# Performance work log

Hardware: AMD Instinct MI355X
Metric: run time of the kernel (lower is better)

## Reference

```python
import jax, jax.numpy as jnp
import numpy as np

N = 50000
DIM = 64
E = 800000


def setup_inputs() -> dict:
    key = jax.random.key(0)
    ks = jax.random.split(key, 12)
    s = 1.0 / np.sqrt(DIM)
    inp = {
        "x": jax.random.normal(ks[0], (N, DIM), dtype=jnp.float32),
        "coord": jax.random.normal(ks[1], (N, DIM), dtype=jnp.float32),
        "Wq": jax.random.uniform(ks[2], (DIM, DIM), jnp.float32, -s, s),
        "bq": jax.random.uniform(ks[3], (DIM,), jnp.float32, -s, s),
        "Wk": jax.random.uniform(ks[4], (DIM, DIM), jnp.float32, -s, s),
        "bk": jax.random.uniform(ks[5], (DIM,), jnp.float32, -s, s),
        "Wv": jax.random.uniform(ks[6], (DIM, DIM), jnp.float32, -s, s),
        "bv": jax.random.uniform(ks[7], (DIM,), jnp.float32, -s, s),
        "Wc": jax.random.uniform(ks[8], (DIM, 1), jnp.float32, -1.0, 1.0),
        "bc": jax.random.uniform(ks[9], (DIM,), jnp.float32, -1.0, 1.0),
        "edge_index": jax.random.randint(ks[10], (2, E), 0, N, dtype=jnp.int64),
    }
    return inp


def reference(x, coord, Wq, bq, Wk, bk, Wv, bv, Wc, bc, edge_index):
    row, col = edge_index[0], edge_index[1]
    # per-edge coordinate differences and distances: [E, DIM], [E, 1]
    dx = coord[row] - coord[col]
    dist = jnp.linalg.norm(dx, axis=-1, keepdims=True)
    # per-edge QKV projections (torch Linear: x @ W.T + b): [E, DIM]
    q = x[row] @ Wq.T + bq
    k = x[col] @ Wk.T + bk
    v = x[col] @ Wv.T + bv
    # scalar attention logit per edge, GLOBAL softmax over all edges (dim=0)
    attn = jnp.sum(q * k, axis=-1, keepdims=True)  # [E, 1]
    weight = jax.nn.softmax(attn, axis=0)          # [E, 1]
    delta_x = weight * v                            # [E, DIM]
    delta_coord = weight * (dist @ Wc.T + bc) * dx  # [E, DIM]
    # scatter-add back to nodes
    x_out = jax.ops.segment_sum(delta_x, row, num_segments=x.shape[0])
    coord_out = jax.ops.segment_sum(delta_coord, row, num_segments=coord.shape[0])
    return (x + x_out, coord + coord_out)
```

## Files before the change

### kernel.cpp

```cpp
#include <hip/hip_runtime.h>
#include <math.h>

#define N_NODES 50000
#define DIM 64
#define NE 800000
#define NSCAN_BLOCKS ((N_NODES + 255) / 256)
#define NFILL_BLOCKS ((NE + 255) / 256)
#define NQKV_BLOCKS ((N_NODES + 31) / 32)

static __device__ __forceinline__ float bf2f(unsigned short u) {
    return __uint_as_float(((unsigned int)u) << 16);
}
static __device__ __forceinline__ unsigned short f2bf(float f) {
    unsigned int u = __float_as_uint(f);
    u += 0x7fffu + ((u >> 16) & 1u);
    return (unsigned short)(u >> 16);
}

typedef float v2f __attribute__((ext_vector_type(2)));
template <bool HI>
static __device__ __forceinline__ v2f fp8x2(unsigned int u) {
    return __builtin_amdgcn_cvt_pk_f32_fp8((int)u, HI);
}
static __device__ __forceinline__ unsigned char f2fp8(float f) {
    int p = __builtin_amdgcn_cvt_pk_fp8_f32(f, f, 0, false);
    return (unsigned char)(p & 0xff);
}


__global__ __launch_bounds__(256, 5) void k_qkv_fill(
    const float* __restrict__ x, const float* __restrict__ coord,
    const float* __restrict__ Wq, const float* __restrict__ bq,
    const float* __restrict__ Wk, const float* __restrict__ bk,
    const float* __restrict__ Wv, const float* __restrict__ bv,
    const int* __restrict__ eidx, int* __restrict__ cursor,
    int* __restrict__ bucket_col,
    float* __restrict__ Qf, unsigned short* __restrict__ KVC)
{
    __shared__ ushort4 WT2[3][1024];
    __shared__ float4  xs4[32][16];

    if (blockIdx.x < NFILL_BLOCKS) {
        int e = blockIdx.x * 256 + threadIdx.x;
        if (e < NE) {
            int pos = atomicAdd(cursor + eidx[e], 1);
            bucket_col[pos] = eidx[NE + e];
        }
        return;
    }

    const int tid  = threadIdx.x;
    const int base = (blockIdx.x - NFILL_BLOCKS) * 32;
    unsigned char* KVB = (unsigned char*)KVC;

    for (int t = tid; t < 1024; t += 256) {
        int d = t & 63, j2 = t >> 6;
        float4 a = ((const float4*)Wq)[d * 16 + j2];
        float4 b = ((const float4*)Wk)[d * 16 + j2];
        float4 c = ((const float4*)Wv)[d * 16 + j2];
        WT2[0][t] = make_ushort4(f2bf(a.x), f2bf(a.y), f2bf(a.z), f2bf(a.w));
        WT2[1][t] = make_ushort4(f2bf(b.x), f2bf(b.y), f2bf(b.z), f2bf(b.w));
        WT2[2][t] = make_ushort4(f2bf(c.x), f2bf(c.y), f2bf(c.z), f2bf(c.w));
    }
    for (int t = tid; t < 32 * DIM; t += 256) {
        int gn = base + (t >> 6);
        if (gn < N_NODES)
            KVB[(size_t)gn * 256 + 192 + (t & 63)] =
                f2fp8(coord[(size_t)gn * DIM + (t & 63)]);
    }
    for (int t = tid; t < 512; t += 256) {
        int r = t >> 4, j2 = t & 15;
        if (base + r < N_NODES)
            xs4[r][j2] = ((const float4*)x)[(size_t)(base + r) * 16 + j2];
    }
    __syncthreads();

    const int wv = tid >> 6;
    const int d  = tid & 63;
    const float bqv = bq[d], bkv = bk[d], bvv = bv[d];

    float aq[8], ak[8], av[8];
    #pragma unroll
    for (int r = 0; r < 8; ++r) { aq[r] = bqv; ak[r] = bkv; av[r] = bvv; }

    #pragma unroll 4
    for (int j2 = 0; j2 < 16; ++j2) {
        ushort4 uq = WT2[0][j2 * 64 + d];
        ushort4 uk = WT2[1][j2 * 64 + d];
        ushort4 uv = WT2[2][j2 * 64 + d];
        float wqx = bf2f(uq.x), wqy = bf2f(uq.y), wqz = bf2f(uq.z), wqw = bf2f(uq.w);
        float wkx = bf2f(uk.x), wky = bf2f(uk.y), wkz = bf2f(uk.z), wkw = bf2f(uk.w);
        float wvx = bf2f(uv.x), wvy = bf2f(uv.y), wvz = bf2f(uv.z), wvw = bf2f(uv.w);
        #pragma unroll
        for (int r = 0; r < 8; ++r) {
            float4 xv = xs4[wv * 8 + r][j2];
            aq[r] += xv.x * wqx + xv.y * wqy + xv.z * wqz + xv.w * wqw;
            ak[r] += xv.x * wkx + xv.y * wky + xv.z * wkz + xv.w * wkw;
            av[r] += xv.x * wvx + xv.y * wvy + xv.z * wvz + xv.w * wvw;
        }
    }
    #pragma unroll
    for (int r = 0; r < 8; ++r) {
        int n = base + wv * 8 + r;
        if (n < N_NODES) {
            Qf[(size_t)n * DIM + d] = aq[r];
            KVC[(size_t)n * 128 + d]       = f2bf(ak[r]);
            KVB[(size_t)n * 256 + 128 + d] = f2fp8(av[r]);
        }
    }
}

__global__ __launch_bounds__(256) void k_hist(
    const int* __restrict__ eidx, int* __restrict__ counts)
{
    int e = blockIdx.x * 256 + threadIdx.x;
    if (e < NE) atomicAdd(counts + eidx[e], 1);
}

__global__ __launch_bounds__(256) void k_scan1(
    const int* __restrict__ counts, int* __restrict__ offsets,
    int* __restrict__ bsums)
{
    __shared__ int tmp[256];
    int i = blockIdx.x * 256 + threadIdx.x;
    int v = (i < N_NODES) ? counts[i] : 0;
    tmp[threadIdx.x] = v;
    __syncthreads();
    #pragma unroll
    for (int off = 1; off < 256; off <<= 1) {
        int t = (threadIdx.x >= off) ? tmp[threadIdx.x - off] : 0;
        __syncthreads();
        tmp[threadIdx.x] += t;
        __syncthreads();
    }
    if (i < N_NODES) offsets[i] = tmp[threadIdx.x] - v;
    if (threadIdx.x == 255) bsums[blockIdx.x] = tmp[255];
}

__global__ __launch_bounds__(256) void k_scan23(
    int* __restrict__ offsets, int* __restrict__ counts,
    const int* __restrict__ bsums)
{
    __shared__ int red[4];
    const int tid = threadIdx.x;
    const int b   = blockIdx.x;
    int v = (tid < b && tid < NSCAN_BLOCKS) ? bsums[tid] : 0;
    #pragma unroll
    for (int off = 32; off; off >>= 1) v += __shfl_xor(v, off);
    if ((tid & 63) == 0) red[tid >> 6] = v;
    __syncthreads();
    const int pre = red[0] + red[1] + red[2] + red[3];

    int i = b * 256 + tid;
    if (i < N_NODES) {
        int o = offsets[i] + pre;
        offsets[i] = o;
        counts[i]  = o;
    }
    if (i == 0) offsets[N_NODES] = NE;
}

__global__ __launch_bounds__(256) void k_edge_fused(
    const int* __restrict__ bucket_col, const int* __restrict__ offsets,
    const float* __restrict__ Qf, const unsigned short* __restrict__ KVC,
    const float* __restrict__ coord,
    const float* __restrict__ Wc, const float* __restrict__ bc,
    float* __restrict__ out_x, float* __restrict__ out_c,
    float* __restrict__ wsum)
{
    const int lane = threadIdx.x & 63;
    const int n = (blockIdx.x * 256 + threadIdx.x) >> 6;
    if (n >= N_NODES) return;
    const int qt = lane >> 4;
    const int sl = lane & 15;

    const float4 q4  = ((const float4*)Qf)[(size_t)n * 16 + sl];
    const float4 cr4 = ((const float4*)coord)[(size_t)n * 16 + sl];
    const float4 wc4 = ((const float4*)Wc)[sl];
    const float4 bc4 = ((const float4*)bc)[sl];
    const ushort4* K16 = (const ushort4*)KVC;
    const unsigned int* U32 = (const unsigned int*)KVC;

    const int s = offsets[n], t = offsets[n + 1];
    float4 accx = {0.f, 0.f, 0.f, 0.f};
    float4 accc = {0.f, 0.f, 0.f, 0.f};
    float psum = 0.0f;

    for (int base = s; base < t; base += 8) {
        int pos0 = base + qt;
        int pos1 = base + 4 + qt;
        bool v0 = pos0 < t, v1 = pos1 < t;
        int c0 = bucket_col[v0 ? pos0 : (t - 1)];
        int c1 = bucket_col[v1 ? pos1 : (t - 1)];
        ushort4      ku0 = K16[(size_t)c0 * 32 + sl];
        unsigned int vu0 = U32[(size_t)c0 * 64 + 32 + sl];
        unsigned int cu0 = U32[(size_t)c0 * 64 + 48 + sl];
        ushort4      ku1 = K16[(size_t)c1 * 32 + sl];
        unsigned int vu1 = U32[(size_t)c1 * 64 + 32 + sl];
        unsigned int cu1 = U32[(size_t)c1 * 64 + 48 + sl];

        v2f c0a = fp8x2<false>(cu0), c0b = fp8x2<true>(cu0);
        v2f c1a = fp8x2<false>(cu1), c1b = fp8x2<true>(cu1);

        float d0 = q4.x * bf2f(ku0.x) + q4.y * bf2f(ku0.y)
                 + q4.z * bf2f(ku0.z) + q4.w * bf2f(ku0.w);
        float dx0x = cr4.x - c0a.x, dx0y = cr4.y - c0a.y;
        float dx0z = cr4.z - c0b.x, dx0w = cr4.w - c0b.y;
        float e0 = dx0x * dx0x + dx0y * dx0y + dx0z * dx0z + dx0w * dx0w;
        float d1 = q4.x * bf2f(ku1.x) + q4.y * bf2f(ku1.y)
                 + q4.z * bf2f(ku1.z) + q4.w * bf2f(ku1.w);
        float dx1x = cr4.x - c1a.x, dx1y = cr4.y - c1a.y;
        float dx1z = cr4.z - c1b.x, dx1w = cr4.w - c1b.y;
        float e1 = dx1x * dx1x + dx1y * dx1y + dx1z * dx1z + dx1w * dx1w;

        #pragma unroll
        for (int off = 1; off <= 8; off <<= 1) {
            d0 += __shfl_xor(d0, off);
            e0 += __shfl_xor(e0, off);
            d1 += __shfl_xor(d1, off);
            e1 += __shfl_xor(e1, off);
        }
        float p0e = v0 ? __expf(d0) : 0.0f;
        float p1e = v1 ? __expf(d1) : 0.0f;
        float dist0 = sqrtf(e0), dist1 = sqrtf(e1);
        psum += p0e + p1e;

        v2f v0a = fp8x2<false>(vu0), v0b = fp8x2<true>(vu0);
        v2f v1a = fp8x2<false>(vu1), v1b = fp8x2<true>(vu1);
        accx.x += p0e * v0a.x + p1e * v1a.x;
        accx.y += p0e * v0a.y + p1e * v1a.y;
        accx.z += p0e * v0b.x + p1e * v1b.x;
        accx.w += p0e * v0b.y + p1e * v1b.y;
        accc.x += p0e * (dist0 * wc4.x + bc4.x) * dx0x
                + p1e * (dist1 * wc4.x + bc4.x) * dx1x;
        accc.y += p0e * (dist0 * wc4.y + bc4.y) * dx0y
                + p1e * (dist1 * wc4.y + bc4.y) * dx1y;
        accc.z += p0e * (dist0 * wc4.z + bc4.z) * dx0z
                + p1e * (dist1 * wc4.z + bc4.z) * dx1z;
        accc.w += p0e * (dist0 * wc4.w + bc4.w) * dx0w
                + p1e * (dist1 * wc4.w + bc4.w) * dx1w;
    }

    #pragma unroll
    for (int off = 16; off <= 32; off <<= 1) {
        accx.x += __shfl_xor(accx.x, off);
        accx.y += __shfl_xor(accx.y, off);
        accx.z += __shfl_xor(accx.z, off);
        accx.w += __shfl_xor(accx.w, off);
        accc.x += __shfl_xor(accc.x, off);
        accc.y += __shfl_xor(accc.y, off);
        accc.z += __shfl_xor(accc.z, off);
        accc.w += __shfl_xor(accc.w, off);
        psum   += __shfl_xor(psum, off);
    }
    if (lane < 16) {
        ((float4*)out_x)[(size_t)n * 16 + sl] = accx;
        ((float4*)out_c)[(size_t)n * 16 + sl] = accc;
    }
    if (lane == 0) wsum[n] = psum;
}

__global__ __launch_bounds__(1024) void k_redsum(
    const float* __restrict__ wsum, float* __restrict__ S)
{
    __shared__ float red[16];
    float a = 0.0f;
    for (int i = threadIdx.x; i < N_NODES; i += 1024) a += wsum[i];
    #pragma unroll
    for (int off = 32; off; off >>= 1) a += __shfl_xor(a, off);
    if ((threadIdx.x & 63) == 0) red[threadIdx.x >> 6] = a;
    __syncthreads();
    if (threadIdx.x == 0) {
        float s = 0.0f;
        #pragma unroll
        for (int w = 0; w < 16; ++w) s += red[w];
        *S = s;
    }
}

__global__ __launch_bounds__(256) void k_finalize(
    const float* __restrict__ x, const float* __restrict__ coord,
    const float* __restrict__ S, float* __restrict__ out)
{
    const float inv = 1.0f / *S;
    const int nd4 = (N_NODES * DIM) / 4;
    const float4* x4 = (const float4*)x;
    const float4* c4 = (const float4*)coord;
    float4* o4 = (float4*)out;
    for (int i = blockIdx.x * 256 + threadIdx.x; i < 2 * nd4;
         i += gridDim.x * 256) {
        float4 r = (i < nd4) ? x4[i] : c4[i - nd4];
        float4 a = o4[i];
        a.x = r.x + a.x * inv;
        a.y = r.y + a.y * inv;
        a.z = r.z + a.z * inv;
        a.w = r.w + a.w * inv;
        o4[i] = a;
    }
}

extern "C" void kernel_launch(void* const* d_in, const int* in_sizes, int n_in,
                              void* d_out, int out_size, void* d_ws, size_t ws_size,
                              hipStream_t stream)
{
    const float* x     = (const float*)d_in[0];
    const float* coord = (const float*)d_in[1];
    const float* Wq    = (const float*)d_in[2];
    const float* bq    = (const float*)d_in[3];
    const float* Wk    = (const float*)d_in[4];
    const float* bk    = (const float*)d_in[5];
    const float* Wv    = (const float*)d_in[6];
    const float* bv    = (const float*)d_in[7];
    const float* Wc    = (const float*)d_in[8];
    const float* bc    = (const float*)d_in[9];
    const int*   eidx  = (const int*)d_in[10];

    float* out = (float*)d_out;
    float* ws  = (float*)d_ws;

    float* Qf = ws;
    unsigned short* KVC = (unsigned short*)(Qf + (size_t)N_NODES * DIM);
    int* bucket_col = (int*)(KVC + (size_t)N_NODES * 128);
    int* counts  = bucket_col + NE;
    int* offsets = counts + N_NODES;
    int* bsums   = offsets + N_NODES + 1;
    float* wsum  = (float*)(bsums + 256);
    float* S     = wsum + N_NODES;

    float* out_x = out;
    float* out_c = out + (size_t)N_NODES * DIM;

    (void)hipMemsetAsync(counts, 0, (size_t)N_NODES * sizeof(int), stream);
    k_hist  <<<(NE + 255) / 256, 256, 0, stream>>>(eidx, counts);
    k_scan1 <<<NSCAN_BLOCKS, 256, 0, stream>>>(counts, offsets, bsums);
    k_scan23<<<NSCAN_BLOCKS, 256, 0, stream>>>(offsets, counts, bsums);

    k_qkv_fill<<<NFILL_BLOCKS + NQKV_BLOCKS, 256, 0, stream>>>(
        x, coord, Wq, bq, Wk, bk, Wv, bv, eidx, counts, bucket_col, Qf, KVC);

    k_edge_fused<<<(N_NODES * 64 + 255) / 256, 256, 0, stream>>>(
        bucket_col, offsets, Qf, KVC, coord, Wc, bc, out_x, out_c, wsum);

    k_redsum<<<1, 1024, 0, stream>>>(wsum, S);
    k_finalize<<<2048, 256, 0, stream>>>(x, coord, S, out);
}
```

Measured before the change: 221.5 us.

## Split fill from QKV kernel and pack fp8 stores into 32-bit words

Separates the edge bucket-fill pass back into its own kernel rather than sharing a grid with the QKV projection. Inside the QKV kernel, coord and V are now converted to fp8 four values at a time and written as 32-bit words. V is staged through shared memory so each thread stores a contiguous packed word, replacing scattered single-byte stores. This cuts the number of narrow global writes, at the cost of an extra kernel launch, two more barriers and lost overlap between fill and QKV.

```diff
diff --git a/kernel.cpp b/kernel.cpp
--- a/kernel.cpp
+++ b/kernel.cpp
@@ -5,8 +5,6 @@
 #define DIM 64
 #define NE 800000
 #define NSCAN_BLOCKS ((N_NODES + 255) / 256)
-#define NFILL_BLOCKS ((NE + 255) / 256)
-#define NQKV_BLOCKS ((N_NODES + 31) / 32)
 
 static __device__ __forceinline__ float bf2f(unsigned short u) {
     return __uint_as_float(((unsigned int)u) << 16);
@@ -22,36 +20,27 @@
 static __device__ __forceinline__ v2f fp8x2(unsigned int u) {
     return __builtin_amdgcn_cvt_pk_f32_fp8((int)u, HI);
 }
-static __device__ __forceinline__ unsigned char f2fp8(float f) {
-    int p = __builtin_amdgcn_cvt_pk_fp8_f32(f, f, 0, false);
-    return (unsigned char)(p & 0xff);
-}
-
-
-__global__ __launch_bounds__(256, 5) void k_qkv_fill(
+static __device__ __forceinline__ unsigned int pack4_fp8(float a, float b,
+                                                         float c, float d) {
+    int p = __builtin_amdgcn_cvt_pk_fp8_f32(a, b, 0, false);
+    p = __builtin_amdgcn_cvt_pk_fp8_f32(c, d, p, true);
+    return (unsigned int)p;
+}
+
+
+__global__ __launch_bounds__(256, 5) void k_qkv(
     const float* __restrict__ x, const float* __restrict__ coord,
     const float* __restrict__ Wq, const float* __restrict__ bq,
     const float* __restrict__ Wk, const float* __restrict__ bk,
     const float* __restrict__ Wv, const float* __restrict__ bv,
-    const int* __restrict__ eidx, int* __restrict__ cursor,
-    int* __restrict__ bucket_col,
     float* __restrict__ Qf, unsigned short* __restrict__ KVC)
 {
     __shared__ ushort4 WT2[3][1024];
     __shared__ float4  xs4[32][16];
 
-    if (blockIdx.x < NFILL_BLOCKS) {
-        int e = blockIdx.x * 256 + threadIdx.x;
-        if (e < NE) {
-            int pos = atomicAdd(cursor + eidx[e], 1);
-            bucket_col[pos] = eidx[NE + e];
-        }
-        return;
-    }
-
     const int tid  = threadIdx.x;
-    const int base = (blockIdx.x - NFILL_BLOCKS) * 32;
-    unsigned char* KVB = (unsigned char*)KVC;
+    const int base = blockIdx.x * 32;
+    unsigned int* U32 = (unsigned int*)KVC;
 
     for (int t = tid; t < 1024; t += 256) {
         int d = t & 63, j2 = t >> 6;
@@ -62,11 +51,12 @@
         WT2[1][t] = make_ushort4(f2bf(b.x), f2bf(b.y), f2bf(b.z), f2bf(b.w));
         WT2[2][t] = make_ushort4(f2bf(c.x), f2bf(c.y), f2bf(c.z), f2bf(c.w));
     }
-    for (int t = tid; t < 32 * DIM; t += 256) {
-        int gn = base + (t >> 6);
-        if (gn < N_NODES)
-            KVB[(size_t)gn * 256 + 192 + (t & 63)] =
-                f2fp8(coord[(size_t)gn * DIM + (t & 63)]);
+    for (int t = tid; t < 512; t += 256) {
+        int n = base + (t >> 4), j = t & 15;
+        if (n < N_NODES) {
+            float4 cv = ((const float4*)coord)[(size_t)n * 16 + j];
+            U32[(size_t)n * 64 + 48 + j] = pack4_fp8(cv.x, cv.y, cv.z, cv.w);
+        }
     }
     for (int t = tid; t < 512; t += 256) {
         int r = t >> 4, j2 = t & 15;
@@ -104,8 +94,21 @@
         int n = base + wv * 8 + r;
         if (n < N_NODES) {
             Qf[(size_t)n * DIM + d] = aq[r];
-            KVC[(size_t)n * 128 + d]       = f2bf(ak[r]);
-            KVB[(size_t)n * 256 + 128 + d] = f2fp8(av[r]);
+            KVC[(size_t)n * 128 + d] = f2bf(ak[r]);
+        }
+    }
+    __syncthreads();
+    float* vf = (float*)xs4;
+    #pragma unroll
+    for (int r = 0; r < 8; ++r)
+        vf[(wv * 8 + r) * 64 + d] = av[r];
+    __syncthreads();
+    for (int t = tid; t < 512; t += 256) {
+        int ln = t >> 4, j = t & 15;
+        int n = base + ln;
+        if (n < N_NODES) {
+            float4 vv = ((const float4*)vf)[ln * 16 + j];
+            U32[(size_t)n * 64 + 32 + j] = pack4_fp8(vv.x, vv.y, vv.z, vv.w);
         }
     }
 }
@@ -158,6 +161,17 @@
         counts[i]  = o;
     }
     if (i == 0) offsets[N_NODES] = NE;
+}
+
+__global__ __launch_bounds__(256) void k_fill(
+    const int* __restrict__ eidx, int* __restrict__ cursor,
+    int* __restrict__ bucket_col)
+{
+    int e = blockIdx.x * 256 + threadIdx.x;
+    if (e < NE) {
+        int pos = atomicAdd(cursor + eidx[e], 1);
+        bucket_col[pos] = eidx[NE + e];
+    }
 }
 
 __global__ __launch_bounds__(256) void k_edge_fused(
@@ -334,9 +348,10 @@
     k_hist  <<<(NE + 255) / 256, 256, 0, stream>>>(eidx, counts);
     k_scan1 <<<NSCAN_BLOCKS, 256, 0, stream>>>(counts, offsets, bsums);
     k_scan23<<<NSCAN_BLOCKS, 256, 0, stream>>>(offsets, counts, bsums);
-
-    k_qkv_fill<<<NFILL_BLOCKS + NQKV_BLOCKS, 256, 0, stream>>>(
-        x, coord, Wq, bq, Wk, bk, Wv, bv, eidx, counts, bucket_col, Qf, KVC);
+    k_fill  <<<(NE + 255) / 256, 256, 0, stream>>>(eidx, counts, bucket_col);
+
+    k_qkv<<<(N_NODES + 31) / 32, 256, 0, stream>>>(
+        x, coord, Wq, bq, Wk, bk, Wv, bv, Qf, KVC);
 
     k_edge_fused<<<(N_NODES * 64 + 255) / 256, 256, 0, stream>>>(
         bucket_col, offsets, Qf, KVC, coord, Wc, bc, out_x, out_c, wsum);
```

New measurement: 218.1 us. Within noise of the previous version (-1.5%).
